# Kernel tuning notes

Hardware: AMD Instinct MI355X
Metric: run time of the kernel (lower is better)

Reference implementation:

```python
import jax, jax.numpy as jnp
import numpy as np

N_NODES = 100000
N_EDGES = 1000000
H = 128  # hidden_size


def setup_inputs() -> dict:
    key = jax.random.key(0)
    ks = jax.random.split(key, 8)
    emb = jax.random.normal(ks[0], (N_NODES, H), dtype=jnp.float32)
    edge_index = jax.random.randint(ks[1], (2, N_EDGES), 0, N_NODES, dtype=jnp.int64)
    # MLP([2H, 4H, H, 1]) weights (Kaiming-ish scaled normals)
    W1 = jax.random.normal(ks[2], (2 * H, 4 * H), dtype=jnp.float32) / np.sqrt(2 * H).astype(np.float32)
    b1 = jnp.zeros((4 * H,), dtype=jnp.float32)
    W2 = jax.random.normal(ks[3], (4 * H, H), dtype=jnp.float32) / np.sqrt(4 * H).astype(np.float32)
    b2 = jnp.zeros((H,), dtype=jnp.float32)
    W3 = jax.random.normal(ks[4], (H, 1), dtype=jnp.float32) / np.sqrt(H).astype(np.float32)
    b3 = jnp.zeros((1,), dtype=jnp.float32)
    return {"emb": emb, "edge_index": edge_index,
            "W1": W1, "b1": b1, "W2": W2, "b2": b2, "W3": W3, "b3": b3}


def reference(emb, edge_index, W1, b1, W2, b2, W3, b3):
    # ExtractorMLP.forward with learn_edge_att=True, eval mode.
    col = edge_index[0]
    row = edge_index[1]
    # edge-gather + concat: [E, 2H]
    f12 = jnp.concatenate([emb[col], emb[row]], axis=-1)
    # MLP([2H, 4H, H, 1]); Dropout is identity in eval mode
    h = jax.nn.relu(f12 @ W1 + b1)          # [E, 4H]
    h = jax.nn.relu(h @ W2 + b2)            # [E, H]
    att_log_logits = h @ W3 + b3            # [E, 1]
    # concrete_sample with training=False -> plain sigmoid
    att = jax.nn.sigmoid(att_log_logits)
    return att
```

## Files before the change

### kernel.cpp

```cpp
#include <hip/hip_runtime.h>
#include <math.h>

#define E_TOTAL   1000000
#define HDIM      128
#define K1        256
#define N1        512
#define N2        128
#define M_TILE    64
#define BLOCK     256

typedef _Float16 f16;
typedef _Float16 f16_4  __attribute__((ext_vector_type(4)));
typedef _Float16 f16_8  __attribute__((ext_vector_type(8)));
typedef float    f32_16 __attribute__((ext_vector_type(16)));

__global__ void prep_weights(const float* __restrict__ W1, const float* __restrict__ W2,
                             f16* __restrict__ W1F, f16* __restrict__ W2F) {
    int t = blockIdx.x * blockDim.x + threadIdx.x;
    const int total1 = K1 * N1;
    const int total2 = N1 * N2;
    if (t < total1) {
        int v    = t & 7;
        int lane = (t >> 3) & 63;
        int kc   = (t >> 9) & 15;
        int nt   = t >> 13;
        int k = kc * 16 + (lane >> 5) * 8 + v;
        int n = nt * 32 + (lane & 31);
        W1F[t] = (f16)W1[k * N1 + n];
    } else if (t < total1 + total2) {
        int u = t - total1;
        int v    = u & 7;
        int lane = (u >> 3) & 63;
        int kcg  = (u >> 9) & 31;
        int nt   = u >> 14;
        int k = kcg * 16 + (lane >> 5) * 8 + v;
        int n = nt * 32 + (lane & 31);
        W2F[u] = (f16)W2[k * N2 + n];
    }
}

__global__ void prep_emb(const float* __restrict__ emb, f16* __restrict__ emb16) {
    int t = blockIdx.x * blockDim.x + threadIdx.x;
    float4 f = ((const float4*)emb)[t];
    f16_4 v = { (f16)f.x, (f16)f.y, (f16)f.z, (f16)f.w };
    ((f16_4*)emb16)[t] = v;
}

template <bool F16EMB>
__global__ __launch_bounds__(BLOCK, 2) void edge_mlp_kernel(
    const float* __restrict__ emb,
    const f16*   __restrict__ emb16,
    const int*   __restrict__ eidx,
    const f16*   __restrict__ W1F,
    const float* __restrict__ b1,
    const f16*   __restrict__ W2F,
    const float* __restrict__ b2,
    const float* __restrict__ W3,
    const float* __restrict__ b3,
    float* __restrict__ out)
{
    __shared__ __align__(16) f16 sBF[2][2 * 8 * 64 * 8];
    __shared__ __align__(16) f16 sH2F[2 * 8 * 64 * 8];

    const int tid  = threadIdx.x;
    const int e0   = blockIdx.x * M_TILE;
    const int wnt  = tid >> 6;
    const int lane = tid & 63;
    const int l31  = lane & 31;
    const int lh   = lane >> 5;

    int node[2][2];
    #pragma unroll
    for (int et = 0; et < 2; ++et)
        #pragma unroll
        for (int side = 0; side < 2; ++side)
            node[et][side] = eidx[side * E_TOTAL + e0 + et * 32 + l31];

    f16_8 ef[2][16];
    if (F16EMB) {
        #pragma unroll
        for (int et = 0; et < 2; ++et)
            #pragma unroll
            for (int kc = 0; kc < 16; ++kc) {
                const f16* src = emb16 + (size_t)node[et][kc >> 3] * HDIM
                                       + (kc & 7) * 16 + lh * 8;
                ef[et][kc] = *(const f16_8*)src;
            }
    } else {
        #pragma unroll
        for (int et = 0; et < 2; ++et)
            #pragma unroll
            for (int kc = 0; kc < 16; ++kc) {
                const float* src = emb + (size_t)node[et][kc >> 3] * HDIM
                                       + (kc & 7) * 16 + lh * 8;
                float4 fa = *(const float4*)(src);
                float4 fb = *(const float4*)(src + 4);
                ef[et][kc] = { (f16)fa.x, (f16)fa.y, (f16)fa.z, (f16)fa.w,
                               (f16)fb.x, (f16)fb.y, (f16)fb.z, (f16)fb.w };
            }
    }

    f32_16 acc2[2] = {{0.f}, {0.f}};

    {
        f32_16 acc1[2] = {{0.f}, {0.f}};
        const int nt = wnt;
        #pragma unroll
        for (int kc = 0; kc < 16; ++kc) {
            f16_8 wf = *(const f16_8*)(W1F + (((nt * 16 + kc) * 64 + lane) << 3));
            #pragma unroll
            for (int et = 0; et < 2; ++et)
                acc1[et] = __builtin_amdgcn_mfma_f32_32x32x16_f16(wf, ef[et][kc], acc1[et], 0, 0, 0);
        }
        f16* bcur = &sBF[0][0];
        #pragma unroll
        for (int et = 0; et < 2; ++et) {
            #pragma unroll
            for (int g = 0; g < 4; ++g) {
                const int wnl = wnt * 32 + lh * 4 + g * 8;
                const float4 bv = *(const float4*)(b1 + wnl);
                f16_4 hv;
                #pragma unroll
                for (int i = 0; i < 4; ++i) {
                    float v = acc1[et][g * 4 + i] + ((const float*)&bv)[i];
                    hv[i] = (f16)(v > 0.f ? v : 0.f);
                }
                const int kl = wnt * 2 + (g >> 1);
                *(f16_4*)(bcur + ((((et * 8 + kl) * 64 + (g & 1) * 32 + l31) << 3) + lh * 4)) = hv;
            }
        }
    }
    __syncthreads();

    #pragma unroll
    for (int q = 1; q < 4; ++q) {
        f32_16 acc1[2] = {{0.f}, {0.f}};
        const int nt = q * 4 + wnt;
        const f16* bprev = &sBF[(q - 1) & 1][0];
        #pragma unroll
        for (int kc = 0; kc < 16; ++kc) {
            f16_8 wf = *(const f16_8*)(W1F + (((nt * 16 + kc) * 64 + lane) << 3));
            #pragma unroll
            for (int et = 0; et < 2; ++et)
                acc1[et] = __builtin_amdgcn_mfma_f32_32x32x16_f16(wf, ef[et][kc], acc1[et], 0, 0, 0);
            if (kc < 8) {
                const int kcg = (q - 1) * 8 + kc;
                f16_8 wf2 = *(const f16_8*)(W2F + (((wnt * 32 + kcg) * 64 + lane) << 3));
                #pragma unroll
                for (int et = 0; et < 2; ++et) {
                    f16_8 ef2 = *(const f16_8*)(bprev + (((et * 8 + kc) * 64 + lane) << 3));
                    acc2[et] = __builtin_amdgcn_mfma_f32_32x32x16_f16(wf2, ef2, acc2[et], 0, 0, 0);
                }
            }
        }
        f16* bcur = &sBF[q & 1][0];
        #pragma unroll
        for (int et = 0; et < 2; ++et) {
            #pragma unroll
            for (int g = 0; g < 4; ++g) {
                const int wnl = wnt * 32 + lh * 4 + g * 8;
                const float4 bv = *(const float4*)(b1 + q * 128 + wnl);
                f16_4 hv;
                #pragma unroll
                for (int i = 0; i < 4; ++i) {
                    float v = acc1[et][g * 4 + i] + ((const float*)&bv)[i];
                    hv[i] = (f16)(v > 0.f ? v : 0.f);
                }
                const int kl = wnt * 2 + (g >> 1);
                *(f16_4*)(bcur + ((((et * 8 + kl) * 64 + (g & 1) * 32 + l31) << 3) + lh * 4)) = hv;
            }
        }
        __syncthreads();
    }

    {
        const f16* bprev = &sBF[1][0];
        #pragma unroll
        for (int kc = 0; kc < 8; ++kc) {
            const int kcg = 24 + kc;
            f16_8 wf2 = *(const f16_8*)(W2F + (((wnt * 32 + kcg) * 64 + lane) << 3));
            #pragma unroll
            for (int et = 0; et < 2; ++et) {
                f16_8 ef2 = *(const f16_8*)(bprev + (((et * 8 + kc) * 64 + lane) << 3));
                acc2[et] = __builtin_amdgcn_mfma_f32_32x32x16_f16(wf2, ef2, acc2[et], 0, 0, 0);
            }
        }
    }

    {
        #pragma unroll
        for (int et = 0; et < 2; ++et) {
            #pragma unroll
            for (int g = 0; g < 4; ++g) {
                const int wn = wnt * 32 + lh * 4 + g * 8;
                const float4 bv = *(const float4*)(b2 + wn);
                f16_4 hv;
                #pragma unroll
                for (int i = 0; i < 4; ++i) {
                    float v = acc2[et][g * 4 + i] + ((const float*)&bv)[i];
                    hv[i] = (f16)(v > 0.f ? v : 0.f);
                }
                const int kl = wnt * 2 + (g >> 1);
                *(f16_4*)(sH2F + ((((et * 8 + kl) * 64 + (g & 1) * 32 + l31) << 3) + lh * 4)) = hv;
            }
        }
    }
    __syncthreads();

    {
        const int m   = tid >> 2;
        const int j   = tid & 3;
        const int met = m >> 5;
        const int m31 = m & 31;
        float s = 0.f;
        #pragma unroll
        for (int jj = 0; jj < 2; ++jj) {
            const int kl = j * 2 + jj;
            f16_8 a = *(const f16_8*)(sH2F + (((met * 8 + kl) * 64 + m31) << 3));
            f16_8 b = *(const f16_8*)(sH2F + (((met * 8 + kl) * 64 + 32 + m31) << 3));
            const float4* w3v = (const float4*)(W3 + kl * 16);
            float4 w0 = w3v[0], w1 = w3v[1], w2 = w3v[2], w3q = w3v[3];
            s += (float)a[0]*w0.x + (float)a[1]*w0.y + (float)a[2]*w0.z + (float)a[3]*w0.w;
            s += (float)a[4]*w1.x + (float)a[5]*w1.y + (float)a[6]*w1.z + (float)a[7]*w1.w;
            s += (float)b[0]*w2.x + (float)b[1]*w2.y + (float)b[2]*w2.z + (float)b[3]*w2.w;
            s += (float)b[4]*w3q.x + (float)b[5]*w3q.y + (float)b[6]*w3q.z + (float)b[7]*w3q.w;
        }
        s += __shfl_xor(s, 1);
        s += __shfl_xor(s, 2);
        if (j == 0) {
            const float logit = s + b3[0];
            out[e0 + m] = 1.0f / (1.0f + __expf(-logit));
        }
    }
}

extern "C" void kernel_launch(void* const* d_in, const int* in_sizes, int n_in,
                              void* d_out, int out_size, void* d_ws, size_t ws_size,
                              hipStream_t stream) {
    const float* emb  = (const float*)d_in[0];
    const int*   eidx = (const int*)d_in[1];
    const float* W1   = (const float*)d_in[2];
    const float* b1   = (const float*)d_in[3];
    const float* W2   = (const float*)d_in[4];
    const float* b2   = (const float*)d_in[5];
    const float* W3   = (const float*)d_in[6];
    const float* b3   = (const float*)d_in[7];
    float* out = (float*)d_out;

    const size_t wbytes   = (size_t)(K1 * N1 + N1 * N2) * sizeof(f16);
    const size_t embbytes = (size_t)100000 * HDIM * sizeof(f16);

    f16* W1F = (f16*)d_ws;
    f16* W2F = W1F + K1 * N1;

    const int prep_total = K1 * N1 + N1 * N2;
    prep_weights<<<(prep_total + 255) / 256, 256, 0, stream>>>(W1, W2, W1F, W2F);

    if (ws_size >= wbytes + embbytes) {
        f16* emb16 = W2F + N1 * N2;
        const int cvt_threads = 100000 * HDIM / 4;
        prep_emb<<<cvt_threads / 256, 256, 0, stream>>>(emb, emb16);
        edge_mlp_kernel<true><<<E_TOTAL / M_TILE, BLOCK, 0, stream>>>(
            emb, emb16, eidx, W1F, b1, W2F, b2, W3, b3, out);
    } else {
        edge_mlp_kernel<false><<<E_TOTAL / M_TILE, BLOCK, 0, stream>>>(
            emb, (const f16*)nullptr, eidx, W1F, b1, W2F, b2, W3, b3, out);
    }
}
```

Before: 663.5 us.

## Give each wave its own 32 edges and fuse layer-2 per wave

The work split changes from four waves sharing 64 edges (each wave computing one slice of the hidden dimension) to each wave owning 32 edges outright and computing the full MLP for them. Layer-1 outputs are staged in a small per-wave LDS buffer and consumed immediately by layer-2 MFMAs. Layer 3 is reduced in registers, which removes most block-wide barriers and the shared H2 staging. The cost is that every wave now streams all of W1 and W2 itself, so per-edge weight traffic rises (cached reads). The change also adds inline-asm gathers with an explicit waitcnt and a tail guard for the partial last block.

```diff
diff --git a/kernel.cpp b/kernel.cpp
--- a/kernel.cpp
+++ b/kernel.cpp
@@ -6,7 +6,7 @@
 #define K1        256
 #define N1        512
 #define N2        128
-#define M_TILE    64
+#define M_TILE    128
 #define BLOCK     256
 
 typedef _Float16 f16;
@@ -59,178 +59,104 @@
     const float* __restrict__ b3,
     float* __restrict__ out)
 {
-    __shared__ __align__(16) f16 sBF[2][2 * 8 * 64 * 8];
-    __shared__ __align__(16) f16 sH2F[2 * 8 * 64 * 8];
+    __shared__ __align__(16) f16 sH[4][2][2][64][8];
 
     const int tid  = threadIdx.x;
-    const int e0   = blockIdx.x * M_TILE;
-    const int wnt  = tid >> 6;
+    const int w    = tid >> 6;
     const int lane = tid & 63;
     const int l31  = lane & 31;
     const int lh   = lane >> 5;
 
-    int node[2][2];
-    #pragma unroll
-    for (int et = 0; et < 2; ++et)
-        #pragma unroll
-        for (int side = 0; side < 2; ++side)
-            node[et][side] = eidx[side * E_TOTAL + e0 + et * 32 + l31];
+    const int e  = blockIdx.x * M_TILE + w * 32 + l31;
+    const int ec = e < E_TOTAL ? e : (E_TOTAL - 1);
 
-    f16_8 ef[2][16];
+    int node[2];
+    node[0] = eidx[ec];
+    node[1] = eidx[E_TOTAL + ec];
+
+    f16_8 ef[16];
     if (F16EMB) {
         #pragma unroll
-        for (int et = 0; et < 2; ++et)
-            #pragma unroll
-            for (int kc = 0; kc < 16; ++kc) {
-                const f16* src = emb16 + (size_t)node[et][kc >> 3] * HDIM
-                                       + (kc & 7) * 16 + lh * 8;
-                ef[et][kc] = *(const f16_8*)src;
-            }
+        for (int kc = 0; kc < 16; ++kc) {
+            const f16* src = emb16 + (size_t)node[kc >> 3] * HDIM + (kc & 7) * 16 + lh * 8;
+            asm volatile("global_load_dwordx4 %0, %1, off" : "=v"(ef[kc]) : "v"(src));
+        }
+        asm volatile("s_waitcnt vmcnt(0)" ::: "memory");
+        __builtin_amdgcn_sched_barrier(0);
     } else {
         #pragma unroll
-        for (int et = 0; et < 2; ++et)
-            #pragma unroll
-            for (int kc = 0; kc < 16; ++kc) {
-                const float* src = emb + (size_t)node[et][kc >> 3] * HDIM
-                                       + (kc & 7) * 16 + lh * 8;
-                float4 fa = *(const float4*)(src);
-                float4 fb = *(const float4*)(src + 4);
-                ef[et][kc] = { (f16)fa.x, (f16)fa.y, (f16)fa.z, (f16)fa.w,
-                               (f16)fb.x, (f16)fb.y, (f16)fb.z, (f16)fb.w };
-            }
+        for (int kc = 0; kc < 16; ++kc) {
+            const float* src = emb + (size_t)node[kc >> 3] * HDIM + (kc & 7) * 16 + lh * 8;
+            float4 fa = *(const float4*)(src);
+            float4 fb = *(const float4*)(src + 4);
+            ef[kc] = { (f16)fa.x, (f16)fa.y, (f16)fa.z, (f16)fa.w,
+                       (f16)fb.x, (f16)fb.y, (f16)fb.z, (f16)fb.w };
+        }
     }
 
-    f32_16 acc2[2] = {{0.f}, {0.f}};
+    f32_16 acc2[4] = {{0.f}, {0.f}, {0.f}, {0.f}};
 
-    {
-        f32_16 acc1[2] = {{0.f}, {0.f}};
-        const int nt = wnt;
+    #pragma unroll
+    for (int ntp = 0; ntp < 8; ++ntp) {
+        f32_16 a1[2] = {{0.f}, {0.f}};
         #pragma unroll
         for (int kc = 0; kc < 16; ++kc) {
-            f16_8 wf = *(const f16_8*)(W1F + (((nt * 16 + kc) * 64 + lane) << 3));
             #pragma unroll
-            for (int et = 0; et < 2; ++et)
-                acc1[et] = __builtin_amdgcn_mfma_f32_32x32x16_f16(wf, ef[et][kc], acc1[et], 0, 0, 0);
+            for (int u = 0; u < 2; ++u) {
+                const int nt = ntp * 2 + u;
+                f16_8 wf = *(const f16_8*)(W1F + (((nt * 16 + kc) * 64 + lane) << 3));
+                a1[u] = __builtin_amdgcn_mfma_f32_32x32x16_f16(wf, ef[kc], a1[u], 0, 0, 0);
+            }
         }
-        f16* bcur = &sBF[0][0];
         #pragma unroll
-        for (int et = 0; et < 2; ++et) {
+        for (int u = 0; u < 2; ++u) {
+            const int nt  = ntp * 2 + u;
+            const int par = u;
             #pragma unroll
             for (int g = 0; g < 4; ++g) {
-                const int wnl = wnt * 32 + lh * 4 + g * 8;
-                const float4 bv = *(const float4*)(b1 + wnl);
+                const float4 bq = *(const float4*)(b1 + nt * 32 + g * 8 + lh * 4);
                 f16_4 hv;
                 #pragma unroll
                 for (int i = 0; i < 4; ++i) {
-                    float v = acc1[et][g * 4 + i] + ((const float*)&bv)[i];
+                    float v = a1[u][g * 4 + i] + ((const float*)&bq)[i];
                     hv[i] = (f16)(v > 0.f ? v : 0.f);
                 }
-                const int kl = wnt * 2 + (g >> 1);
-                *(f16_4*)(bcur + ((((et * 8 + kl) * 64 + (g & 1) * 32 + l31) << 3) + lh * 4)) = hv;
+                *(f16_4*)(&sH[w][par][g >> 1][(g & 1) * 32 + l31][lh * 4]) = hv;
+            }
+            #pragma unroll
+            for (int c = 0; c < 2; ++c) {
+                f16_8 hf = *(const f16_8*)(&sH[w][par][c][lane][0]);
+                const int kcg = nt * 2 + c;
+                #pragma unroll
+                for (int n2 = 0; n2 < 4; ++n2) {
+                    f16_8 wf2 = *(const f16_8*)(W2F + (((n2 * 32 + kcg) * 64 + lane) << 3));
+                    acc2[n2] = __builtin_amdgcn_mfma_f32_32x32x16_f16(wf2, hf, acc2[n2], 0, 0, 0);
+                }
+            }
+        }
+        if ((ntp & 1) == 1 && ntp != 7) __builtin_amdgcn_s_barrier();
+    }
+
+    float s = 0.f;
+    #pragma unroll
+    for (int n2 = 0; n2 < 4; ++n2) {
+        #pragma unroll
+        for (int g = 0; g < 4; ++g) {
+            const int off = n2 * 32 + g * 8 + lh * 4;
+            const float4 b2q = *(const float4*)(b2 + off);
+            const float4 w3q = *(const float4*)(W3 + off);
+            #pragma unroll
+            for (int i = 0; i < 4; ++i) {
+                float v = acc2[n2][g * 4 + i] + ((const float*)&b2q)[i];
+                v = v > 0.f ? v : 0.f;
+                s += v * ((const float*)&w3q)[i];
             }
         }
     }
-    __syncthreads();
-
-    #pragma unroll
-    for (int q = 1; q < 4; ++q) {
-        f32_16 acc1[2] = {{0.f}, {0.f}};
-        const int nt = q * 4 + wnt;
-        const f16* bprev = &sBF[(q - 1) & 1][0];
-        #pragma unroll
-        for (int kc = 0; kc < 16; ++kc) {
-            f16_8 wf = *(const f16_8*)(W1F + (((nt * 16 + kc) * 64 + lane) << 3));
-            #pragma unroll
-            for (int et = 0; et < 2; ++et)
-                acc1[et] = __builtin_amdgcn_mfma_f32_32x32x16_f16(wf, ef[et][kc], acc1[et], 0, 0, 0);
-            if (kc < 8) {
-                const int kcg = (q - 1) * 8 + kc;
-                f16_8 wf2 = *(const f16_8*)(W2F + (((wnt * 32 + kcg) * 64 + lane) << 3));
-                #pragma unroll
-                for (int et = 0; et < 2; ++et) {
-                    f16_8 ef2 = *(const f16_8*)(bprev + (((et * 8 + kc) * 64 + lane) << 3));
-                    acc2[et] = __builtin_amdgcn_mfma_f32_32x32x16_f16(wf2, ef2, acc2[et], 0, 0, 0);
-                }
-            }
-        }
-        f16* bcur = &sBF[q & 1][0];
-        #pragma unroll
-        for (int et = 0; et < 2; ++et) {
-            #pragma unroll
-            for (int g = 0; g < 4; ++g) {
-                const int wnl = wnt * 32 + lh * 4 + g * 8;
-                const float4 bv = *(const float4*)(b1 + q * 128 + wnl);
-                f16_4 hv;
-                #pragma unroll
-                for (int i = 0; i < 4; ++i) {
-                    float v = acc1[et][g * 4 + i] + ((const float*)&bv)[i];
-                    hv[i] = (f16)(v > 0.f ? v : 0.f);
-                }
-                const int kl = wnt * 2 + (g >> 1);
-                *(f16_4*)(bcur + ((((et * 8 + kl) * 64 + (g & 1) * 32 + l31) << 3) + lh * 4)) = hv;
-            }
-        }
-        __syncthreads();
-    }
-
-    {
-        const f16* bprev = &sBF[1][0];
-        #pragma unroll
-        for (int kc = 0; kc < 8; ++kc) {
-            const int kcg = 24 + kc;
-            f16_8 wf2 = *(const f16_8*)(W2F + (((wnt * 32 + kcg) * 64 + lane) << 3));
-            #pragma unroll
-            for (int et = 0; et < 2; ++et) {
-                f16_8 ef2 = *(const f16_8*)(bprev + (((et * 8 + kc) * 64 + lane) << 3));
-                acc2[et] = __builtin_amdgcn_mfma_f32_32x32x16_f16(wf2, ef2, acc2[et], 0, 0, 0);
-            }
-        }
-    }
-
-    {
-        #pragma unroll
-        for (int et = 0; et < 2; ++et) {
-            #pragma unroll
-            for (int g = 0; g < 4; ++g) {
-                const int wn = wnt * 32 + lh * 4 + g * 8;
-                const float4 bv = *(const float4*)(b2 + wn);
-                f16_4 hv;
-                #pragma unroll
-                for (int i = 0; i < 4; ++i) {
-                    float v = acc2[et][g * 4 + i] + ((const float*)&bv)[i];
-                    hv[i] = (f16)(v > 0.f ? v : 0.f);
-                }
-                const int kl = wnt * 2 + (g >> 1);
-                *(f16_4*)(sH2F + ((((et * 8 + kl) * 64 + (g & 1) * 32 + l31) << 3) + lh * 4)) = hv;
-            }
-        }
-    }
-    __syncthreads();
-
-    {
-        const int m   = tid >> 2;
-        const int j   = tid & 3;
-        const int met = m >> 5;
-        const int m31 = m & 31;
-        float s = 0.f;
-        #pragma unroll
-        for (int jj = 0; jj < 2; ++jj) {
-            const int kl = j * 2 + jj;
-            f16_8 a = *(const f16_8*)(sH2F + (((met * 8 + kl) * 64 + m31) << 3));
-            f16_8 b = *(const f16_8*)(sH2F + (((met * 8 + kl) * 64 + 32 + m31) << 3));
-            const float4* w3v = (const float4*)(W3 + kl * 16);
-            float4 w0 = w3v[0], w1 = w3v[1], w2 = w3v[2], w3q = w3v[3];
-            s += (float)a[0]*w0.x + (float)a[1]*w0.y + (float)a[2]*w0.z + (float)a[3]*w0.w;
-            s += (float)a[4]*w1.x + (float)a[5]*w1.y + (float)a[6]*w1.z + (float)a[7]*w1.w;
-            s += (float)b[0]*w2.x + (float)b[1]*w2.y + (float)b[2]*w2.z + (float)b[3]*w2.w;
-            s += (float)b[4]*w3q.x + (float)b[5]*w3q.y + (float)b[6]*w3q.z + (float)b[7]*w3q.w;
-        }
-        s += __shfl_xor(s, 1);
-        s += __shfl_xor(s, 2);
-        if (j == 0) {
-            const float logit = s + b3[0];
-            out[e0 + m] = 1.0f / (1.0f + __expf(-logit));
-        }
+    s += __shfl_xor(s, 32);
+    if (lh == 0 && e < E_TOTAL) {
+        const float logit = s + b3[0];
+        out[e] = 1.0f / (1.0f + __expf(-logit));
     }
 }
 
@@ -256,14 +182,16 @@
     const int prep_total = K1 * N1 + N1 * N2;
     prep_weights<<<(prep_total + 255) / 256, 256, 0, stream>>>(W1, W2, W1F, W2F);
 
+    const int nblocks = (E_TOTAL + M_TILE - 1) / M_TILE;
+
     if (ws_size >= wbytes + embbytes) {
         f16* emb16 = W2F + N1 * N2;
         const int cvt_threads = 100000 * HDIM / 4;
         prep_emb<<<cvt_threads / 256, 256, 0, stream>>>(emb, emb16);
-        edge_mlp_kernel<true><<<E_TOTAL / M_TILE, BLOCK, 0, stream>>>(
+        edge_mlp_kernel<true><<<nblocks, BLOCK, 0, stream>>>(
             emb, emb16, eidx, W1F, b1, W2F, b2, W3, b3, out);
     } else {
-        edge_mlp_kernel<false><<<E_TOTAL / M_TILE, BLOCK, 0, stream>>>(
+        edge_mlp_kernel<false><<<nblocks, BLOCK, 0, stream>>>(
             emb, (const f16*)nullptr, eidx, W1F, b1, W2F, b2, W3, b3, out);
     }
 }
```

Result: slower. 1.609 ms (+142.5%).
